# Optimization experiments

Hardware: AMD Instinct MI355X
Metric: run time of the kernel (lower is better)

The kernel has to match this reference:

```python
import jax, jax.numpy as jnp
import numpy as np

BS, DEMO_DIM, FEAT_DIM = 16384, 32, 256


def setup_inputs() -> dict:
    key = jax.random.key(0)
    k1, k2, k3 = jax.random.split(key, 3)
    x = jax.random.normal(k1, (BS, DEMO_DIM), dtype=jnp.float32)
    # Stacked per-index Linear(1, feat_dim) params: W[i, f] = weight of proj i, b[i, f] = bias
    W = jax.random.normal(k2, (DEMO_DIM, FEAT_DIM), dtype=jnp.float32)
    b = jax.random.normal(k3, (DEMO_DIM, FEAT_DIM), dtype=jnp.float32)
    return {"x": x, "W": W, "b": b}


def reference(x, W, b):
    # out[b, i, f] = x[b, i] * W[i, f] + b[i, f]  -- fused broadcasted multiply-add
    return x[:, :, None] * W[None, :, :] + b[None, :, :]
```

## Files before the change

kernel.cpp:

```cpp
#include <hip/hip_runtime.h>


#define BS_N      16384
#define DEMO_DIM  32
#define FEAT_DIM  256

typedef float vf4 __attribute__((ext_vector_type(4)));

__global__ __launch_bounds__(256) void demoproj_kernel(
    const float* __restrict__ x,
    const float* __restrict__ W,
    const float* __restrict__ B,
    float* __restrict__ out)
{
    const size_t g = (size_t)blockIdx.x * blockDim.x + threadIdx.x;
    const size_t e = g << 2;
    const int    f = (int)(e & (FEAT_DIM - 1));
    const size_t row = e >> 8;
    const int    i = (int)(row & (DEMO_DIM - 1));

    const float xv = x[row];

    const vf4 wv = *reinterpret_cast<const vf4*>(W + (size_t)i * FEAT_DIM + f);
    const vf4 bv = *reinterpret_cast<const vf4*>(B + (size_t)i * FEAT_DIM + f);

    vf4 o;
    o.x = fmaf(xv, wv.x, bv.x);
    o.y = fmaf(xv, wv.y, bv.y);
    o.z = fmaf(xv, wv.z, bv.z);
    o.w = fmaf(xv, wv.w, bv.w);

    reinterpret_cast<vf4*>(out)[g] = o;
}

extern "C" void kernel_launch(void* const* d_in, const int* in_sizes, int n_in,
                              void* d_out, int out_size, void* d_ws, size_t ws_size,
                              hipStream_t stream) {
    const float* x = (const float*)d_in[0];
    const float* W = (const float*)d_in[1];
    const float* B = (const float*)d_in[2];
    float* out = (float*)d_out;

    const size_t total_f4 = (size_t)BS_N * DEMO_DIM * FEAT_DIM / 4;
    const int block = 256;
    const int grid = (int)(total_f4 / block);

    demoproj_kernel<<<grid, block, 0, stream>>>(x, W, B, out);
}
```

Measured before the change: 558.7 us.

## Use persistent wave-per-row loop keeping W and b in registers

Replaces the one-thread-per-vec4 launch with a fixed grid of 2048 blocks in which each wave loops over rows sharing the same demo index. The wave loads its W and b slice into registers once and only reloads the scalar x per iteration. This cuts redundant W/b loads and block scheduling overhead on a store-bound kernel. The fixed grid may underuse the GPU or change how stores interleave across memory channels.

```diff
diff --git a/kernel.cpp b/kernel.cpp
--- a/kernel.cpp
+++ b/kernel.cpp
@@ -4,6 +4,10 @@
 #define BS_N      16384
 #define DEMO_DIM  32
 #define FEAT_DIM  256
+#define NROWS     (BS_N * DEMO_DIM)
+#define NBLOCKS   2048
+#define NWAVES    (NBLOCKS * 4)
+#define ITERS     (NROWS / NWAVES)
 
 typedef float vf4 __attribute__((ext_vector_type(4)));
 
@@ -13,24 +17,28 @@
     const float* __restrict__ B,
     float* __restrict__ out)
 {
-    const size_t g = (size_t)blockIdx.x * blockDim.x + threadIdx.x;
-    const size_t e = g << 2;
-    const int    f = (int)(e & (FEAT_DIM - 1));
-    const size_t row = e >> 8;
-    const int    i = (int)(row & (DEMO_DIM - 1));
+    const int lane = threadIdx.x & 63;
+    const int wv   = blockIdx.x * 4 + (threadIdx.x >> 6);
+    const int f    = lane << 2;
+    const int i    = wv & (DEMO_DIM - 1);
 
-    const float xv = x[row];
+    const vf4 wreg = *reinterpret_cast<const vf4*>(W + (size_t)i * FEAT_DIM + f);
+    const vf4 breg = *reinterpret_cast<const vf4*>(B + (size_t)i * FEAT_DIM + f);
 
-    const vf4 wv = *reinterpret_cast<const vf4*>(W + (size_t)i * FEAT_DIM + f);
-    const vf4 bv = *reinterpret_cast<const vf4*>(B + (size_t)i * FEAT_DIM + f);
+    size_t r = (size_t)wv;
+    float* o0 = out + (size_t)wv * FEAT_DIM + f;
+    const size_t ostride = (size_t)NWAVES * FEAT_DIM;
 
-    vf4 o;
-    o.x = fmaf(xv, wv.x, bv.x);
-    o.y = fmaf(xv, wv.y, bv.y);
-    o.z = fmaf(xv, wv.z, bv.z);
-    o.w = fmaf(xv, wv.w, bv.w);
-
-    reinterpret_cast<vf4*>(out)[g] = o;
+    #pragma unroll 4
+    for (int k = 0; k < ITERS; ++k, r += NWAVES, o0 += ostride) {
+        const float xv = x[r];
+        vf4 o;
+        o.x = fmaf(xv, wreg.x, breg.x);
+        o.y = fmaf(xv, wreg.y, breg.y);
+        o.z = fmaf(xv, wreg.z, breg.z);
+        o.w = fmaf(xv, wreg.w, breg.w);
+        *reinterpret_cast<vf4*>(o0) = o;
+    }
 }
 
 extern "C" void kernel_launch(void* const* d_in, const int* in_sizes, int n_in,
@@ -41,9 +49,5 @@
     const float* B = (const float*)d_in[2];
     float* out = (float*)d_out;
 
-    const size_t total_f4 = (size_t)BS_N * DEMO_DIM * FEAT_DIM / 4;
-    const int block = 256;
-    const int grid = (int)(total_f4 / block);
-
-    demoproj_kernel<<<grid, block, 0, stream>>>(x, W, B, out);
+    demoproj_kernel<<<NBLOCKS, 256, 0, stream>>>(x, W, B, out);
 }
```

Result: faster. 545.5 us (-2.4%).
